# Kernel optimization log

Measured on AMD Instinct MI355X. Metric: run time of the kernel, lower is better.

Reference implementation:

```python
import jax, jax.numpy as jnp
import numpy as np

LOG_SCALE_INIT = float(np.log(10.0))


def lorentz_linear(x, W, b, log_scale):
    # nonlin (gelu) -> linear -> Lorentz time/space renormalization
    y = jax.nn.gelu(x) @ W.T + b
    time = jax.nn.sigmoid(y[..., :1]) * jnp.exp(log_scale) + 1.1
    nar = y[..., 1:]
    denom = jnp.clip(jnp.sum(nar * nar, axis=-1, keepdims=True), 1e-8, None)
    scale = (time * time - 1.0) / denom
    return jnp.concatenate([time, nar * jnp.sqrt(scale)], axis=-1)


def ffn_lorentz(x, W1, b1, s1, W2, b2, s2):
    return lorentz_linear(lorentz_linear(x, W1, b1, s1), W2, b2, s2) + x


def knn_indices(x, k):
    # x: (B,N,C). KNN on detached features (as in ViG dense_knn_matrix).
    xs = jax.lax.stop_gradient(x)
    sq = jnp.sum(xs * xs, axis=-1)  # (B,N)
    d = sq[:, :, None] + sq[:, None, :] - 2.0 * jnp.einsum('bnc,bmc->bnm', xs, xs)
    _, idx = jax.lax.top_k(-d, k)  # (B,N,k) nearest (includes self)
    return idx


def graph_conv(x, Wg, bg, sg, k):
    # Max-relative graph conv with Lorentz linear. x: (B,N,C)
    idx = knn_indices(x, k)
    xj = jax.vmap(lambda xb, ib: xb[ib])(x, idx)  # (B,N,k,C) gather
    msg = jnp.max(xj - x[:, :, None, :], axis=2)  # (B,N,C)
    h = jnp.concatenate([x, msg], axis=-1)        # (B,N,2C)
    return lorentz_linear(h, Wg, bg, sg)


def setup_inputs() -> dict:
    key = jax.random.key(0)
    ks = jax.random.split(key, 8)
    B, C, H, W = 8, 192, 56, 56
    x = jax.random.normal(ks[0], (B, C, H, W), dtype=jnp.float32)
    def lin(k_, fin, fout):
        return jax.random.normal(k_, (fout, fin), dtype=jnp.float32) * 0.02
    p = {
        'x': x,
        'W1': lin(ks[1], C, C), 'b1': jnp.zeros((C,), jnp.float32), 's1': jnp.float32(LOG_SCALE_INIT),
        'W2': lin(ks[2], C, C), 'b2': jnp.zeros((C,), jnp.float32), 's2': jnp.float32(LOG_SCALE_INIT),
        'Wg': lin(ks[3], 2 * C, C), 'bg': jnp.zeros((C,), jnp.float32), 'sg': jnp.float32(LOG_SCALE_INIT),
        'W3': lin(ks[4], C, C), 'b3': jnp.zeros((C,), jnp.float32), 's3': jnp.float32(LOG_SCALE_INIT),
        'W4': lin(ks[5], C, C), 'b4': jnp.zeros((C,), jnp.float32), 's4': jnp.float32(LOG_SCALE_INIT),
        'k': 9,
    }
    return p


def reference(x, W1, b1, s1, W2, b2, s2, Wg, bg, sg, W3, b3, s3, W4, b4, s4, k):
    B, C, H, W = x.shape
    xn = x.reshape(B, C, H * W).transpose(0, 2, 1)  # (B,N,C) == rearrange b c (h w) 1 -> b (h w) c
    shortcut = xn
    xn = ffn_lorentz(xn, W1, b1, s1, W2, b2, s2)
    xn = graph_conv(xn, Wg, bg, sg, k)
    xn = ffn_lorentz(xn, W3, b3, s3, W4, b4, s4)
    xn = xn + shortcut  # drop_path = 0 -> identity
    return xn.transpose(0, 2, 1).reshape(B, C, H, W)
```

## Files before the change

### kernel.cpp

```cpp
#include <hip/hip_runtime.h>
#include <math.h>

#define NB   8
#define NC   192
#define NPIX 3136
#define NPAD 3200
#define GRID_LL (NB*98)
#define NIT  25
#define NSP  8
#define GRID_KNN (NB*NIT*NSP)
#define GRID_MSG (NB*196)
#define FINF 3.4e38f

typedef _Float16 f16x8 __attribute__((ext_vector_type(8)));
typedef float   f32x16 __attribute__((ext_vector_type(16)));

__device__ __forceinline__ float gelu_f(float x){
    float u = 0.7978845608028654f * (x + 0.044715f * x * x * x);
    return 0.5f * x * (1.0f + tanhf(u));
}

__device__ __forceinline__ unsigned pack_hi(float a, float b){
    union { _Float16 f; unsigned short u; } ha, hb;
    ha.f = (_Float16)a; hb.f = (_Float16)b;
    return (unsigned)ha.u | ((unsigned)hb.u << 16);
}

#define LESS9(da,ia,db,ib) ((da) < (db) || ((da) == (db) && (ia) < (ib)))
#define CSW9(a,ia,b,ib) { bool sw_ = LESS9(b,ib,a,ia); float tf_=(a); int ti_=(ia); \
    (a) = sw_? (b) : (a); (ia) = sw_? (ib) : (ia); (b) = sw_? tf_ : (b); (ib) = sw_? ti_ : (ib); }

struct Top9 {
    float d0,d1,d2,d3,d4,d5,d6,d7,d8;
    int   j0,j1,j2,j3,j4,j5,j6,j7,j8;
    __device__ __forceinline__ void init(){
        d0=d1=d2=d3=d4=d5=d6=d7=d8=FINF;
        j0=j1=j2=j3=j4=j5=j6=j7=j8=0x7FFFFFFF;
    }
    __device__ __forceinline__ void insert(float nd, int ni){
        if (!LESS9(nd, ni, d8, j8)) return;
        d8 = nd; j8 = ni;
        CSW9(d7,j7,d8,j8); CSW9(d6,j6,d7,j7); CSW9(d5,j5,d6,j6); CSW9(d4,j4,d5,j5);
        CSW9(d3,j3,d4,j4); CSW9(d2,j2,d3,j3); CSW9(d1,j1,d2,j2); CSW9(d0,j0,d1,j1);
    }
};

__device__ __forceinline__ unsigned f2mono(float e){
    unsigned u = __float_as_uint(e);
    return u ^ ((unsigned)((int)u >> 31) | 0x80000000u);
}
__device__ __forceinline__ float unmono(unsigned m){
    return __uint_as_float(m ^ ((unsigned)(((int)~m) >> 31) | 0x80000000u));
}

#define CSK(a,b) { unsigned h_ = (a) > (b) ? (a) : (b); unsigned l_ = (a) > (b) ? (b) : (a); (a) = h_; (b) = l_; }
#define INSKEY(x_) if ((x_) > t_k11){ t_k11 = (x_); \
    CSK(t_k10,t_k11) CSK(t_k9,t_k10) CSK(t_k8,t_k9) CSK(t_k7,t_k8) \
    CSK(t_k6,t_k7) CSK(t_k5,t_k6) CSK(t_k4,t_k5) CSK(t_k3,t_k4) \
    CSK(t_k2,t_k3) CSK(t_k1,t_k2) CSK(t_k0,t_k1) }

#define KQ(A,Q) { \
    unsigned q0_ = (f2mono(A[4*(Q)+0]) & 0xFFFFF000u) | (unsigned)(jinvb_ - 8*(Q)    ); \
    unsigned q1_ = (f2mono(A[4*(Q)+1]) & 0xFFFFF000u) | (unsigned)(jinvb_ - 8*(Q) - 1); \
    unsigned q2_ = (f2mono(A[4*(Q)+2]) & 0xFFFFF000u) | (unsigned)(jinvb_ - 8*(Q) - 2); \
    unsigned q3_ = (f2mono(A[4*(Q)+3]) & 0xFFFFF000u) | (unsigned)(jinvb_ - 8*(Q) - 3); \
    unsigned qa_ = q0_ > q1_ ? q0_ : q1_; \
    unsigned qb_ = q2_ > q3_ ? q2_ : q3_; \
    unsigned qm_ = qa_ > qb_ ? qa_ : qb_; \
    if (qm_ > t_k11){ INSKEY(q0_) INSKEY(q1_) INSKEY(q2_) INSKEY(q3_) } }

#define AMAX16(A) fmaxf(fmaxf(fmaxf(fmaxf(A[0],A[1]),fmaxf(A[2],A[3])),fmaxf(fmaxf(A[4],A[5]),fmaxf(A[6],A[7]))), \
                        fmaxf(fmaxf(fmaxf(A[8],A[9]),fmaxf(A[10],A[11])),fmaxf(fmaxf(A[12],A[13]),fmaxf(A[14],A[15]))))

#define INSACCK(A,JS) { float am_ = AMAX16(A); \
    if (am_ >= thrf){ int jinvb_ = 4095 - (jg + (JS)*32 + 4*h); \
        KQ(A,0) KQ(A,1) KQ(A,2) KQ(A,3) } }

#define MF(ACC,AO,BO) ACC = __builtin_amdgcn_mfma_f32_32x32x16_f16(AO,BO,ACC,0,0,0);
#define ZERO16 {0,0,0,0,0,0,0,0,0,0,0,0,0,0,0,0}

__global__ __launch_bounds__(256) void wt_kernel(
    const float* __restrict__ W1, const float* __restrict__ W2,
    const float* __restrict__ Wg, const float* __restrict__ W3,
    const float* __restrict__ W4,
    float* __restrict__ W1T, float* __restrict__ W2T, float* __restrict__ WgT,
    float* __restrict__ W3T, float* __restrict__ W4T)
{
    __shared__ float tile[32*33];
    int t = blockIdx.x;
    const float* src; float* dst; int Kin;
    if (t < 36)      { src = W1; dst = W1T; Kin = 192; }
    else if (t < 72) { src = W2; dst = W2T; Kin = 192; t -= 36; }
    else if (t < 144){ src = Wg; dst = WgT; Kin = 384; t -= 72; }
    else if (t < 180){ src = W3; dst = W3T; Kin = 192; t -= 144; }
    else             { src = W4; dst = W4T; Kin = 192; t -= 180; }
    int ntc = Kin >> 5;
    int tr = t / ntc, tc = t - tr*ntc;
    int tid = threadIdx.x;
    {
        int i = tid >> 3, j4 = (tid & 7)*4;
        float4 v = *(const float4*)&src[(size_t)(tr*32 + i)*Kin + tc*32 + j4];
        tile[i*33 + j4+0] = v.x; tile[i*33 + j4+1] = v.y;
        tile[i*33 + j4+2] = v.z; tile[i*33 + j4+3] = v.w;
    }
    __syncthreads();
    {
        int j = tid >> 3, i4 = (tid & 7)*4;
        float4 o = make_float4(tile[(i4+0)*33 + j], tile[(i4+1)*33 + j],
                               tile[(i4+2)*33 + j], tile[(i4+3)*33 + j]);
        *(float4*)&dst[(size_t)(tc*32 + j)*192 + tr*32 + i4] = o;
    }
}

__global__ __launch_bounds__(256) void pad_kernel(
    unsigned short* __restrict__ Xh, unsigned short* __restrict__ S2h)
{
    const int b = blockIdx.x;
    const int tid = threadIdx.x;
    uint4 z = make_uint4(0,0,0,0);
    for (int e = tid; e < 1536; e += 256){
        int r = e / 24, c8 = (e % 24) * 8;
        *(uint4*)&Xh[((size_t)b*NPAD + NPIX + r)*192 + c8] = z;
    }
    if (tid < 64){
        union { _Float16 f; unsigned short u; } p;
        p.f = (_Float16)(-30000.0f);
        S2h[(size_t)b*NPAD + NPIX + tid] = p.u;
    }
}

template<int K, bool DUAL, bool AX, bool AR, bool CONVF>
__global__ __launch_bounds__(256, 4) void ll2_kernel(
    const float* __restrict__ A0, const float* __restrict__ A1,
    const float* __restrict__ WT, const float* __restrict__ bias,
    const float* __restrict__ sptr, const float* __restrict__ Xres,
    const float* __restrict__ Rcm,
    float* __restrict__ OutCM, float* __restrict__ Hrm,
    unsigned short* __restrict__ Xh, unsigned short* __restrict__ S2h,
    float* __restrict__ SQf)
{
    __shared__ float lA[32*36];
    __shared__ float lW[32*196];

    const int tid = threadIdx.x;
    const int tx = tid & 15, ty = tid >> 4;
    const int bid = blockIdx.x;
    const int b  = bid / 98;
    const int n0 = (bid % 98) * 32;

    float acc[2][12];
    #pragma unroll
    for (int mi = 0; mi < 2; ++mi)
        #pragma unroll
        for (int j = 0; j < 12; ++j) acc[mi][j] = 0.f;

    for (int kt = 0; kt < K/32; ++kt){
        {
            int kk = tid >> 3;
            int m4 = (tid & 7) * 4;
            int c  = kt*32 + kk;
            const float* pl;
            if (K > 192 && c >= 192) pl = A1 + ((size_t)b*192 + (c - 192))*NPIX;
            else                     pl = A0 + ((size_t)b*192 + c)*NPIX;
            float4 v = *(const float4*)&pl[n0 + m4];
            v.x = gelu_f(v.x); v.y = gelu_f(v.y); v.z = gelu_f(v.z); v.w = gelu_f(v.w);
            *(float4*)&lA[kk*36 + m4] = v;
        }
        #pragma unroll
        for (int r = 0; r < 6; ++r){
            int e  = tid + r*256;
            int kk = e / 48;
            int c4 = (e - kk*48) * 4;
            float4 v = *(const float4*)&WT[(size_t)(kt*32 + kk)*192 + c4];
            *(float4*)&lW[kk*196 + c4] = v;
        }
        __syncthreads();
        #pragma unroll
        for (int kk = 0; kk < 32; ++kk){
            float2 a2 = *(const float2*)&lA[kk*36 + ty*2];
            float4 w0 = *(const float4*)&lW[kk*196 + tx*12];
            float4 w1 = *(const float4*)&lW[kk*196 + tx*12 + 4];
            float4 w2 = *(const float4*)&lW[kk*196 + tx*12 + 8];
            float aw[2]  = {a2.x, a2.y};
            float wv[12] = {w0.x,w0.y,w0.z,w0.w, w1.x,w1.y,w1.z,w1.w, w2.x,w2.y,w2.z,w2.w};
            #pragma unroll
            for (int mi = 0; mi < 2; ++mi)
                #pragma unroll
                for (int j = 0; j < 12; ++j)
                    acc[mi][j] = fmaf(aw[mi], wv[j], acc[mi][j]);
        }
        __syncthreads();
    }

    const int lane = tid & 63;
    float es = expf(sptr[0]);
    float bv[12];
    #pragma unroll
    for (int q = 0; q < 3; ++q){
        float4 t4 = *(const float4*)&bias[tx*12 + q*4];
        bv[q*4+0] = t4.x; bv[q*4+1] = t4.y; bv[q*4+2] = t4.z; bv[q*4+3] = t4.w;
    }
    #pragma unroll
    for (int mi = 0; mi < 2; ++mi){
        float part = 0.f;
        #pragma unroll
        for (int j = 0; j < 12; ++j){
            float y = acc[mi][j] + bv[j];
            acc[mi][j] = y;
            if (!(tx == 0 && j == 0)) part += y * y;
        }
        #pragma unroll
        for (int m = 1; m < 16; m <<= 1) part += __shfl_xor(part, m, 64);
        float y0   = __shfl(acc[mi][0], lane & 48, 64);
        float tval = es / (1.f + expf(-y0)) + 1.1f;
        float denom = fmaxf(part, 1e-8f);
        float sca  = (tval*tval - 1.f) / denom;
        float sqs  = sqrtf(sca);
        #pragma unroll
        for (int j = 0; j < 12; ++j){
            float o = acc[mi][j] * sqs;
            if (tx == 0 && j == 0) o = tval;
            acc[mi][j] = o;
        }
    }
    if (AX){
        #pragma unroll
        for (int j = 0; j < 12; ++j){
            int c = tx*12 + j;
            float2 xv = *(const float2*)&Xres[((size_t)b*192 + c)*NPIX + n0 + ty*2];
            acc[0][j] += xv.x; acc[1][j] += xv.y;
        }
    }
    if (AR){
        #pragma unroll
        for (int j = 0; j < 12; ++j){
            int c = tx*12 + j;
            float2 rv = *(const float2*)&Rcm[((size_t)b*192 + c)*NPIX + n0 + ty*2];
            acc[0][j] += rv.x; acc[1][j] += rv.y;
        }
    }
    #pragma unroll
    for (int j = 0; j < 12; ++j){
        int c = tx*12 + j;
        *(float2*)&OutCM[((size_t)b*192 + c)*NPIX + n0 + ty*2] = make_float2(acc[0][j], acc[1][j]);
    }
    if (DUAL){
        #pragma unroll
        for (int mi = 0; mi < 2; ++mi){
            #pragma unroll
            for (int q = 0; q < 3; ++q){
                float4 o = make_float4(acc[mi][q*4+0], acc[mi][q*4+1], acc[mi][q*4+2], acc[mi][q*4+3]);
                *(float4*)&Hrm[((size_t)b*NPIX + n0 + ty*2 + mi)*192 + tx*12 + q*4] = o;
            }
        }
    }
    if (CONVF){
        #pragma unroll
        for (int mi = 0; mi < 2; ++mi){
            int row = n0 + ty*2 + mi;
            float s = 0.f;
            #pragma unroll
            for (int j = 0; j < 12; ++j) s = fmaf(acc[mi][j], acc[mi][j], s);
            #pragma unroll
            for (int m = 1; m < 16; m <<= 1) s += __shfl_xor(s, m, 64);
            #pragma unroll
            for (int q = 0; q < 3; ++q){
                uint2 hv;
                hv.x = pack_hi(acc[mi][q*4+0], acc[mi][q*4+1]);
                hv.y = pack_hi(acc[mi][q*4+2], acc[mi][q*4+3]);
                *(uint2*)&Xh[((size_t)b*NPAD + row)*192 + tx*12 + q*4] = hv;
            }
            if (tx == 0){
                SQf[(size_t)b*NPIX + row] = s;
                union { _Float16 f; unsigned short u; } hh;
                hh.f = (_Float16)(-0.5f * s);
                S2h[(size_t)b*NPAD + row] = hh.u;
            }
        }
    }
}

__global__ __launch_bounds__(256) __attribute__((amdgpu_waves_per_eu(2))) void knn_kernel(
    const unsigned short* __restrict__ Xh, const unsigned short* __restrict__ S2h,
    unsigned* __restrict__ PK)
{
    __shared__ uint4 lds[1280];

    const int tid  = threadIdx.x;
    const int lane = tid & 63;
    const int w    = tid >> 6;
    const int l31  = lane & 31;
    const int h    = lane >> 5;
    const int bid  = blockIdx.x;
    const int b    = bid & 7;
    const int t2   = bid >> 3;
    const int itile = t2 >> 3;
    const int sp    = t2 & 7;
    const int i0    = itile * 128;
    const int g0 = (sp*25)/NSP, g1 = ((sp+1)*25)/NSP;
    const size_t rowb = (size_t)b * NPAD;

    unsigned t_k0=0,t_k1=0,t_k2=0,t_k3=0,t_k4=0,t_k5=0,
             t_k6=0,t_k7=0,t_k8=0,t_k9=0,t_k10=0,t_k11=0;
    float thrf = -FINF;

    for (int g = g0; g < g1; ++g){
        const int jg = g*128;
        f32x16 acc0 = ZERO16, acc1 = ZERO16, acc2 = ZERO16, acc3 = ZERO16;

        for (int kc = 0; kc < 6; ++kc){
            __syncthreads();
            #pragma unroll
            for (int rr = 0; rr < 4; ++rr){
                int u   = tid + rr*256;
                int arr = u >> 9;
                int rs  = (u >> 2) & 127;
                int seg = u & 3;
                int row = (arr == 0) ? (jg + rs) : (i0 + rs);
                uint4 v = *(const uint4*)&Xh[(rowb + row)*192 + kc*32 + seg*8];
                lds[arr*640 + rs*5 + seg] = v;
            }
            __syncthreads();
            #pragma unroll
            for (int ks = 0; ks < 2; ++ks){
                int kq  = ks*2 + h;
                int rb  = l31*5 + kq;
                f16x8 bh = __builtin_bit_cast(f16x8, lds[640 + w*160 + rb]);
                f16x8 a0h = __builtin_bit_cast(f16x8, lds[  0 + rb]);
                f16x8 a1h = __builtin_bit_cast(f16x8, lds[160 + rb]);
                f16x8 a2h = __builtin_bit_cast(f16x8, lds[320 + rb]);
                f16x8 a3h = __builtin_bit_cast(f16x8, lds[480 + rb]);
                MF(acc0, a0h, bh)
                MF(acc1, a1h, bh)
                MF(acc2, a2h, bh)
                MF(acc3, a3h, bh)
            }
        }

        {
            unsigned m  = (h == 0) ? 0xFFFFFFFFu : 0u;
            unsigned om = 0x3C00u & m;
            f16x8 one = __builtin_bit_cast(f16x8, make_uint4(om, 0, 0, 0));
            unsigned s0 = (unsigned)S2h[rowb + jg +  0 + l31];
            unsigned s1 = (unsigned)S2h[rowb + jg + 32 + l31];
            unsigned s2 = (unsigned)S2h[rowb + jg + 64 + l31];
            unsigned s3 = (unsigned)S2h[rowb + jg + 96 + l31];
            f16x8 a;
            a = __builtin_bit_cast(f16x8, make_uint4(s0 & m, 0,0,0)); MF(acc0, a, one)
            a = __builtin_bit_cast(f16x8, make_uint4(s1 & m, 0,0,0)); MF(acc1, a, one)
            a = __builtin_bit_cast(f16x8, make_uint4(s2 & m, 0,0,0)); MF(acc2, a, one)
            a = __builtin_bit_cast(f16x8, make_uint4(s3 & m, 0,0,0)); MF(acc3, a, one)
        }

        INSACCK(acc0, 0)
        INSACCK(acc1, 1)
        INSACCK(acc2, 2)
        INSACCK(acc3, 3)
        thrf = (t_k11 != 0u) ? unmono(t_k11 & 0xFFFFF000u) : -FINF;
    }

    #define MRGK(Kk) { unsigned ok_ = __shfl((int)(Kk), lane ^ 32, 64); \
                      if (lane < 32) { INSKEY((unsigned)ok_) } }
    MRGK(t_k0) MRGK(t_k1) MRGK(t_k2) MRGK(t_k3) MRGK(t_k4) MRGK(t_k5)
    MRGK(t_k6) MRGK(t_k7) MRGK(t_k8) MRGK(t_k9) MRGK(t_k10) MRGK(t_k11)

    if (lane < 32){
        size_t po = ((size_t)(t2*8 + b)*128 + (size_t)w*32 + l31)*12;
        PK[po+ 0] = t_k0;  PK[po+ 1] = t_k1;  PK[po+ 2] = t_k2;  PK[po+ 3] = t_k3;
        PK[po+ 4] = t_k4;  PK[po+ 5] = t_k5;  PK[po+ 6] = t_k6;  PK[po+ 7] = t_k7;
        PK[po+ 8] = t_k8;  PK[po+ 9] = t_k9;  PK[po+10] = t_k10; PK[po+11] = t_k11;
    }
}

__global__ __launch_bounds__(256) void merge_msg_kernel(
    const float* __restrict__ H, const float* __restrict__ SQf,
    const unsigned* __restrict__ PK, float* __restrict__ Msg)
{
    __shared__ float liX[16*196];
    __shared__ unsigned kv[1600];
    __shared__ float cd[256];
    __shared__ int   cidx[256];
    __shared__ int   fidx[144];

    const int tid = threadIdx.x;
    const int bid = blockIdx.x;
    const int b  = bid / 196;
    const int i0 = (bid % 196) * 16;
    const int base = b * NPIX;

    #pragma unroll
    for (int k = 0; k < 3; ++k){
        int f = tid + k*256;
        int r = f / 48, c4 = f % 48;
        *(float4*)&liX[r*196 + c4*4] = *(const float4*)&H[(size_t)(base + i0 + r)*192 + c4*4];
    }
    if (tid < 128){
        int r = tid >> 3, sp = tid & 7;
        int i = i0 + r;
        size_t po = ((size_t)(((i>>7)*NSP + sp)*8 + b)*128 + (i & 127))*12;
        #pragma unroll
        for (int q = 0; q < 3; ++q)
            *(uint4*)&kv[r*100 + sp*12 + q*4] = *(const uint4*)&PK[po + q*4];
    }
    __syncthreads();

    if (tid < 16){
        int r = tid;
        int h0=0,h1=0,h2=0,h3=0,h4=0,h5=0,h6=0,h7=0;
        #pragma unroll
        for (int p = 0; p < 16; ++p){
            unsigned bk = 0; int bs = 0;
#define HEADC(SP,HV) { \
            unsigned k_ = (HV < 12) ? kv[r*100 + SP*12 + HV] : 0u; \
            bool bt_ = k_ > bk; \
            bk = bt_? k_ : bk; bs = bt_? SP : bs; }
            HEADC(0,h0) HEADC(1,h1) HEADC(2,h2) HEADC(3,h3)
            HEADC(4,h4) HEADC(5,h5) HEADC(6,h6) HEADC(7,h7)
#undef HEADC
            cidx[r*16 + p] = 4095 - (int)(bk & 0xFFFu);
            h0 += (bs==0); h1 += (bs==1); h2 += (bs==2); h3 += (bs==3);
            h4 += (bs==4); h5 += (bs==5); h6 += (bs==6); h7 += (bs==7);
        }
    }
    __syncthreads();

    {
        int r = tid >> 4, p = tid & 15;
        int j = cidx[r*16 + p];
        const float* hj = &H[(size_t)(base + j)*192];
        float dot = 0.f;
        #pragma unroll
        for (int q = 0; q < 48; ++q){
            float4 xv = *(const float4*)&liX[r*196 + q*4];
            float4 yv = *(const float4*)&hj[q*4];
            dot = fmaf(xv.x,yv.x, fmaf(xv.y,yv.y, fmaf(xv.z,yv.z, fmaf(xv.w,yv.w, dot))));
        }
        cd[r*16 + p] = SQf[base + j] - 2.f*dot;
    }
    __syncthreads();

    if (tid < 16){
        int r = tid;
        Top9 m; m.init();
        #pragma unroll
        for (int c = 0; c < 16; ++c) m.insert(cd[r*16 + c], cidx[r*16 + c]);
        fidx[r*9+0]=m.j0; fidx[r*9+1]=m.j1; fidx[r*9+2]=m.j2; fidx[r*9+3]=m.j3;
        fidx[r*9+4]=m.j4; fidx[r*9+5]=m.j5; fidx[r*9+6]=m.j6; fidx[r*9+7]=m.j7;
        fidx[r*9+8]=m.j8;
    }
    __syncthreads();

    int rr = tid & 15, part = tid >> 4;
    int ii = i0 + rr;
    int nbr[9];
    #pragma unroll
    for (int e = 0; e < 9; ++e) nbr[e] = fidx[rr*9 + e];
    #pragma unroll
    for (int q = 0; q < 3; ++q){
        float4 mv = make_float4(-FINF, -FINF, -FINF, -FINF);
        #pragma unroll
        for (int e = 0; e < 9; ++e){
            float4 v = *(const float4*)&H[(size_t)(base + nbr[e])*192 + part*12 + q*4];
            mv.x = fmaxf(mv.x, v.x); mv.y = fmaxf(mv.y, v.y);
            mv.z = fmaxf(mv.z, v.z); mv.w = fmaxf(mv.w, v.w);
        }
        float4 xi = *(const float4*)&liX[rr*196 + part*12 + q*4];
        float m0 = mv.x - xi.x, m1 = mv.y - xi.y, m2 = mv.z - xi.z, m3 = mv.w - xi.w;
        int c = part*12 + q*4;
        Msg[((size_t)b*192 + c+0)*NPIX + ii] = m0;
        Msg[((size_t)b*192 + c+1)*NPIX + ii] = m1;
        Msg[((size_t)b*192 + c+2)*NPIX + ii] = m2;
        Msg[((size_t)b*192 + c+3)*NPIX + ii] = m3;
    }
}

extern "C" void kernel_launch(void* const* d_in, const int* in_sizes, int n_in,
                              void* d_out, int out_size, void* d_ws, size_t ws_size,
                              hipStream_t stream)
{
    const float* x  = (const float*)d_in[0];
    const float* W1 = (const float*)d_in[1];
    const float* b1 = (const float*)d_in[2];
    const float* s1 = (const float*)d_in[3];
    const float* W2 = (const float*)d_in[4];
    const float* b2 = (const float*)d_in[5];
    const float* s2 = (const float*)d_in[6];
    const float* Wg = (const float*)d_in[7];
    const float* bg = (const float*)d_in[8];
    const float* sg = (const float*)d_in[9];
    const float* W3 = (const float*)d_in[10];
    const float* b3 = (const float*)d_in[11];
    const float* s3 = (const float*)d_in[12];
    const float* W4 = (const float*)d_in[13];
    const float* b4 = (const float*)d_in[14];
    const float* s4 = (const float*)d_in[15];

    const size_t PL = (size_t)25088*192;
    float* Hrm  = (float*)d_ws;
    float* X1cm = Hrm  + PL;
    float* T1cm = X1cm + PL;
    float* X2cm = T1cm + PL;
    float* MXr  = X2cm + PL;
    unsigned short* Xh = (unsigned short*)MXr;
    float* Msg = MXr;
    unsigned short* S2h = (unsigned short*)(MXr + PL);
    float* SQf = (float*)(S2h + (size_t)NB*NPAD);
    float* W1T = SQf + (size_t)NB*NPIX;
    float* W2T = W1T + 36864;
    float* WgT = W2T + 36864;
    float* W3T = WgT + 73728;
    float* W4T = W3T + 36864;
    unsigned* PK = (unsigned*)X2cm;
    float* out = (float*)d_out;

    wt_kernel<<<216, 256, 0, stream>>>(W1, W2, Wg, W3, W4, W1T, W2T, WgT, W3T, W4T);
    pad_kernel<<<NB, 256, 0, stream>>>(Xh, S2h);
    ll2_kernel<192, false, false, false, false><<<GRID_LL, 256, 0, stream>>>(x,    x,    W1T, b1, s1, nullptr, nullptr, T1cm, nullptr, nullptr, nullptr, nullptr);
    ll2_kernel<192, true , true , false, true ><<<GRID_LL, 256, 0, stream>>>(T1cm, T1cm, W2T, b2, s2, x,       nullptr, X1cm, Hrm, Xh, S2h, SQf);
    knn_kernel<<<GRID_KNN, 256, 0, stream>>>(Xh, S2h, PK);
    merge_msg_kernel<<<GRID_MSG, 256, 0, stream>>>(Hrm, SQf, PK, Msg);
    ll2_kernel<384, false, false, false, false><<<GRID_LL, 256, 0, stream>>>(X1cm, Msg,  WgT, bg, sg, nullptr, nullptr, X2cm, nullptr, nullptr, nullptr, nullptr);
    ll2_kernel<192, false, false, false, false><<<GRID_LL, 256, 0, stream>>>(X2cm, X2cm, W3T, b3, s3, nullptr, nullptr, T1cm, nullptr, nullptr, nullptr, nullptr);
    ll2_kernel<192, false, true , true , false><<<GRID_LL, 256, 0, stream>>>(T1cm, T1cm, W4T, b4, s4, x,       X2cm,    out,  nullptr, nullptr, nullptr, nullptr);
}
```

Measured before the change: 501.3 us.

## Move post-KNN Lorentz linears to split-fp16 MFMA kernels with row-major activations

Adds an MFMA-based Lorentz linear kernel that uses hi/lo fp16 splitting (three MFMAs per step) to keep near-fp32 accuracy, and uses it for the graph-conv, W3 and W4 layers in place of the scalar fp32 ll2 kernel. Intermediate activations move to row-major layout, and the message kernel now writes row-major float4 instead of strided channel-major scalars. The W3 output is stored pre-gelu'd and split into fp16 hi/lo so the next layer can load it directly. This trades extra MFMA work and a weight-split pre-pass for removing the slow FMA GEMMs, and accepts some precision risk from the fp16 split.

```diff
diff --git a/kernel.cpp b/kernel.cpp
--- a/kernel.cpp
+++ b/kernel.cpp
@@ -5,7 +5,8 @@
 #define NC   192
 #define NPIX 3136
 #define NPAD 3200
-#define GRID_LL (NB*98)
+#define NMT  98
+#define GRID_LL (NB*NMT)
 #define NIT  25
 #define NSP  8
 #define GRID_KNN (NB*NIT*NSP)
@@ -19,11 +20,11 @@
     float u = 0.7978845608028654f * (x + 0.044715f * x * x * x);
     return 0.5f * x * (1.0f + tanhf(u));
 }
-
+__device__ __forceinline__ unsigned short h2u(_Float16 v){
+    union { _Float16 f; unsigned short u; } c; c.f = v; return c.u;
+}
 __device__ __forceinline__ unsigned pack_hi(float a, float b){
-    union { _Float16 f; unsigned short u; } ha, hb;
-    ha.f = (_Float16)a; hb.f = (_Float16)b;
-    return (unsigned)ha.u | ((unsigned)hb.u << 16);
+    return (unsigned)h2u((_Float16)a) | ((unsigned)h2u((_Float16)b) << 16);
 }
 
 #define LESS9(da,ia,db,ib) ((da) < (db) || ((da) == (db) && (ia) < (ib)))
@@ -81,25 +82,17 @@
 
 __global__ __launch_bounds__(256) void wt_kernel(
     const float* __restrict__ W1, const float* __restrict__ W2,
-    const float* __restrict__ Wg, const float* __restrict__ W3,
-    const float* __restrict__ W4,
-    float* __restrict__ W1T, float* __restrict__ W2T, float* __restrict__ WgT,
-    float* __restrict__ W3T, float* __restrict__ W4T)
+    float* __restrict__ W1T, float* __restrict__ W2T)
 {
     __shared__ float tile[32*33];
     int t = blockIdx.x;
-    const float* src; float* dst; int Kin;
-    if (t < 36)      { src = W1; dst = W1T; Kin = 192; }
-    else if (t < 72) { src = W2; dst = W2T; Kin = 192; t -= 36; }
-    else if (t < 144){ src = Wg; dst = WgT; Kin = 384; t -= 72; }
-    else if (t < 180){ src = W3; dst = W3T; Kin = 192; t -= 144; }
-    else             { src = W4; dst = W4T; Kin = 192; t -= 180; }
-    int ntc = Kin >> 5;
-    int tr = t / ntc, tc = t - tr*ntc;
+    const float* src; float* dst;
+    if (t < 36){ src = W1; dst = W1T; } else { src = W2; dst = W2T; t -= 36; }
+    int tr = t / 6, tc = t - tr*6;
     int tid = threadIdx.x;
     {
         int i = tid >> 3, j4 = (tid & 7)*4;
-        float4 v = *(const float4*)&src[(size_t)(tr*32 + i)*Kin + tc*32 + j4];
+        float4 v = *(const float4*)&src[(size_t)(tr*32 + i)*192 + tc*32 + j4];
         tile[i*33 + j4+0] = v.x; tile[i*33 + j4+1] = v.y;
         tile[i*33 + j4+2] = v.z; tile[i*33 + j4+3] = v.w;
     }
@@ -112,6 +105,23 @@
     }
 }
 
+__global__ __launch_bounds__(256) void wt16_kernel(
+    const float* __restrict__ Wg, const float* __restrict__ W3,
+    const float* __restrict__ W4,
+    unsigned short* __restrict__ Wh, unsigned short* __restrict__ Wl)
+{
+    int i = blockIdx.x*256 + threadIdx.x;
+    if (i >= 147456) return;
+    const float* src; int off;
+    if (i < 73728)       { src = Wg; off = i; }
+    else if (i < 110592) { src = W3; off = i - 73728; }
+    else                 { src = W4; off = i - 110592; }
+    float w = src[off];
+    _Float16 hi = (_Float16)w;
+    Wh[i] = h2u(hi);
+    Wl[i] = h2u((_Float16)(w - (float)hi));
+}
+
 __global__ __launch_bounds__(256) void pad_kernel(
     unsigned short* __restrict__ Xh, unsigned short* __restrict__ S2h)
 {
@@ -129,12 +139,11 @@
     }
 }
 
-template<int K, bool DUAL, bool AX, bool AR, bool CONVF>
+template<int K, bool WCM, bool DUAL, bool AX, bool CONVF>
 __global__ __launch_bounds__(256, 4) void ll2_kernel(
     const float* __restrict__ A0, const float* __restrict__ A1,
     const float* __restrict__ WT, const float* __restrict__ bias,
     const float* __restrict__ sptr, const float* __restrict__ Xres,
-    const float* __restrict__ Rcm,
     float* __restrict__ OutCM, float* __restrict__ Hrm,
     unsigned short* __restrict__ Xh, unsigned short* __restrict__ S2h,
     float* __restrict__ SQf)
@@ -145,8 +154,8 @@
     const int tid = threadIdx.x;
     const int tx = tid & 15, ty = tid >> 4;
     const int bid = blockIdx.x;
-    const int b  = bid / 98;
-    const int n0 = (bid % 98) * 32;
+    const int b  = bid / NMT;
+    const int n0 = (bid % NMT) * 32;
 
     float acc[2][12];
     #pragma unroll
@@ -231,18 +240,12 @@
             acc[0][j] += xv.x; acc[1][j] += xv.y;
         }
     }
-    if (AR){
+    if (WCM){
         #pragma unroll
         for (int j = 0; j < 12; ++j){
             int c = tx*12 + j;
-            float2 rv = *(const float2*)&Rcm[((size_t)b*192 + c)*NPIX + n0 + ty*2];
-            acc[0][j] += rv.x; acc[1][j] += rv.y;
-        }
-    }
-    #pragma unroll
-    for (int j = 0; j < 12; ++j){
-        int c = tx*12 + j;
-        *(float2*)&OutCM[((size_t)b*192 + c)*NPIX + n0 + ty*2] = make_float2(acc[0][j], acc[1][j]);
+            *(float2*)&OutCM[((size_t)b*192 + c)*NPIX + n0 + ty*2] = make_float2(acc[0][j], acc[1][j]);
+        }
     }
     if (DUAL){
         #pragma unroll
@@ -272,10 +275,146 @@
             }
             if (tx == 0){
                 SQf[(size_t)b*NPIX + row] = s;
-                union { _Float16 f; unsigned short u; } hh;
-                hh.f = (_Float16)(-0.5f * s);
-                S2h[(size_t)b*NPAD + row] = hh.u;
+                S2h[(size_t)b*NPAD + row] = h2u((_Float16)(-0.5f * s));
             }
+        }
+    }
+}
+
+template<int K, int AMODE, bool ESPL, bool EF32, bool AXCM, bool ARRM, bool OUTCM>
+__global__ __launch_bounds__(192) void mll_kernel(
+    const unsigned short* __restrict__ Ash, const unsigned short* __restrict__ Asl,
+    const float* __restrict__ Af0, const float* __restrict__ Af1,
+    const unsigned short* __restrict__ Wh, const unsigned short* __restrict__ Wl,
+    const float* __restrict__ bias, const float* __restrict__ sptr,
+    const float* __restrict__ Xcm, const float* __restrict__ Rrm,
+    float* __restrict__ OutF,
+    unsigned short* __restrict__ Oh, unsigned short* __restrict__ Ol)
+{
+    __shared__ float psum[3][32], y0v[32];
+    const int tid = threadIdx.x;
+    const int w = tid >> 6, lane = tid & 63, l31 = lane & 31, h = lane >> 5;
+    const int bid = blockIdx.x;
+    const int b = bid / NMT, mt = bid % NMT;
+    const int row0 = mt*32;
+    const int nb = w*64;
+    const size_t arow = (size_t)b*NPIX + row0 + l31;
+    const int c0 = nb + l31, c1 = nb + 32 + l31;
+
+    f32x16 acc0 = ZERO16, acc1 = ZERO16;
+
+    #pragma unroll
+    for (int ks = 0; ks < K/16; ++ks){
+        const int kb = ks*16 + h*8;
+        f16x8 ah, al;
+        if (AMODE == 0){
+            ah = __builtin_bit_cast(f16x8, *(const uint4*)&Ash[arow*192 + kb]);
+            al = __builtin_bit_cast(f16x8, *(const uint4*)&Asl[arow*192 + kb]);
+        } else {
+            const float* src;
+            if (AMODE == 2) src = (ks < 12) ? (Af0 + arow*192 + kb) : (Af1 + arow*192 + (kb - 192));
+            else            src = Af0 + arow*192 + kb;
+            float4 f0 = *(const float4*)src;
+            float4 f1 = *(const float4*)(src + 4);
+            float g[8] = {f0.x,f0.y,f0.z,f0.w,f1.x,f1.y,f1.z,f1.w};
+            #pragma unroll
+            for (int e = 0; e < 8; ++e){
+                float gg = gelu_f(g[e]);
+                _Float16 hi = (_Float16)gg;
+                ah[e] = hi;
+                al[e] = (_Float16)(gg - (float)hi);
+            }
+        }
+        f16x8 wh0 = __builtin_bit_cast(f16x8, *(const uint4*)&Wh[(size_t)c0*K + kb]);
+        f16x8 wl0 = __builtin_bit_cast(f16x8, *(const uint4*)&Wl[(size_t)c0*K + kb]);
+        f16x8 wh1 = __builtin_bit_cast(f16x8, *(const uint4*)&Wh[(size_t)c1*K + kb]);
+        f16x8 wl1 = __builtin_bit_cast(f16x8, *(const uint4*)&Wl[(size_t)c1*K + kb]);
+        MF(acc0, ah, wh0) MF(acc0, al, wh0) MF(acc0, ah, wl0)
+        MF(acc1, ah, wh1) MF(acc1, al, wh1) MF(acc1, ah, wl1)
+    }
+
+    const float es = expf(sptr[0]);
+    const float bv0 = bias[c0], bv1 = bias[c1];
+    float o0[16], o1[16], p[16];
+    #pragma unroll
+    for (int r = 0; r < 16; ++r){
+        o0[r] = acc0[r] + bv0;
+        o1[r] = acc1[r] + bv1;
+        p[r] = o0[r]*o0[r] + o1[r]*o1[r];
+    }
+    #pragma unroll
+    for (int m = 1; m < 32; m <<= 1){
+        #pragma unroll
+        for (int r = 0; r < 16; ++r) p[r] += __shfl_xor(p[r], m, 64);
+    }
+    if (l31 == 0){
+        #pragma unroll
+        for (int r = 0; r < 16; ++r){
+            int row = (r&3) + 8*(r>>2) + 4*h;
+            float v = p[r];
+            if (w == 0){ v -= o0[r]*o0[r]; y0v[row] = o0[r]; }
+            psum[w][row] = v;
+        }
+    }
+    __syncthreads();
+    #pragma unroll
+    for (int r = 0; r < 16; ++r){
+        int row = (r&3) + 8*(r>>2) + 4*h;
+        float S = psum[0][row] + psum[1][row] + psum[2][row];
+        float y0 = y0v[row];
+        float tval = es / (1.f + expf(-y0)) + 1.1f;
+        float denom = fmaxf(S, 1e-8f);
+        float sqs = sqrtf((tval*tval - 1.f)/denom);
+        o0[r] *= sqs; o1[r] *= sqs;
+        if (w == 0 && l31 == 0) o0[r] = tval;
+    }
+    if (AXCM){
+        #pragma unroll
+        for (int p4 = 0; p4 < 4; ++p4){
+            float4 xv0 = *(const float4*)&Xcm[((size_t)b*192 + c0)*NPIX + row0 + 8*p4 + 4*h];
+            float4 xv1 = *(const float4*)&Xcm[((size_t)b*192 + c1)*NPIX + row0 + 8*p4 + 4*h];
+            o0[4*p4+0] += xv0.x; o0[4*p4+1] += xv0.y; o0[4*p4+2] += xv0.z; o0[4*p4+3] += xv0.w;
+            o1[4*p4+0] += xv1.x; o1[4*p4+1] += xv1.y; o1[4*p4+2] += xv1.z; o1[4*p4+3] += xv1.w;
+        }
+    }
+    if (ARRM){
+        #pragma unroll
+        for (int r = 0; r < 16; ++r){
+            int row = (r&3) + 8*(r>>2) + 4*h;
+            o0[r] += Rrm[((size_t)b*NPIX + row0 + row)*192 + c0];
+            o1[r] += Rrm[((size_t)b*NPIX + row0 + row)*192 + c1];
+        }
+    }
+    if (OUTCM){
+        #pragma unroll
+        for (int p4 = 0; p4 < 4; ++p4){
+            *(float4*)&OutF[((size_t)b*192 + c0)*NPIX + row0 + 8*p4 + 4*h] =
+                make_float4(o0[4*p4+0], o0[4*p4+1], o0[4*p4+2], o0[4*p4+3]);
+            *(float4*)&OutF[((size_t)b*192 + c1)*NPIX + row0 + 8*p4 + 4*h] =
+                make_float4(o1[4*p4+0], o1[4*p4+1], o1[4*p4+2], o1[4*p4+3]);
+        }
+    }
+    if (EF32){
+        #pragma unroll
+        for (int r = 0; r < 16; ++r){
+            int row = (r&3) + 8*(r>>2) + 4*h;
+            OutF[((size_t)b*NPIX + row0 + row)*192 + c0] = o0[r];
+            OutF[((size_t)b*NPIX + row0 + row)*192 + c1] = o1[r];
+        }
+    }
+    if (ESPL){
+        #pragma unroll
+        for (int r = 0; r < 16; ++r){
+            int row = (r&3) + 8*(r>>2) + 4*h;
+            size_t o = ((size_t)b*NPIX + row0 + row)*192;
+            float g0 = gelu_f(o0[r]);
+            _Float16 h0 = (_Float16)g0;
+            Oh[o + c0] = h2u(h0);
+            Ol[o + c0] = h2u((_Float16)(g0 - (float)h0));
+            float g1 = gelu_f(o1[r]);
+            _Float16 h1 = (_Float16)g1;
+            Oh[o + c1] = h2u(h1);
+            Ol[o + c1] = h2u((_Float16)(g1 - (float)h1));
         }
     }
 }
@@ -450,7 +589,7 @@
     }
     __syncthreads();
 
-    int rr = tid & 15, part = tid >> 4;
+    int rr = tid >> 4, part = tid & 15;
     int ii = i0 + rr;
     int nbr[9];
     #pragma unroll
@@ -465,12 +604,8 @@
             mv.z = fmaxf(mv.z, v.z); mv.w = fmaxf(mv.w, v.w);
         }
         float4 xi = *(const float4*)&liX[rr*196 + part*12 + q*4];
-        float m0 = mv.x - xi.x, m1 = mv.y - xi.y, m2 = mv.z - xi.z, m3 = mv.w - xi.w;
-        int c = part*12 + q*4;
-        Msg[((size_t)b*192 + c+0)*NPIX + ii] = m0;
-        Msg[((size_t)b*192 + c+1)*NPIX + ii] = m1;
-        Msg[((size_t)b*192 + c+2)*NPIX + ii] = m2;
-        Msg[((size_t)b*192 + c+3)*NPIX + ii] = m3;
+        *(float4*)&Msg[(size_t)(base + ii)*192 + part*12 + q*4] =
+            make_float4(mv.x - xi.x, mv.y - xi.y, mv.z - xi.z, mv.w - xi.w);
     }
 }
 
@@ -494,32 +629,44 @@
     const float* W4 = (const float*)d_in[13];
     const float* b4 = (const float*)d_in[14];
     const float* s4 = (const float*)d_in[15];
-
-    const size_t PL = (size_t)25088*192;
-    float* Hrm  = (float*)d_ws;
-    float* X1cm = Hrm  + PL;
-    float* T1cm = X1cm + PL;
-    float* X2cm = T1cm + PL;
-    float* MXr  = X2cm + PL;
-    unsigned short* Xh = (unsigned short*)MXr;
-    float* Msg = MXr;
-    unsigned short* S2h = (unsigned short*)(MXr + PL);
+    float* ws = (float*)d_ws;
+    float* out = (float*)d_out;
+
+    const size_t NE = (size_t)NB*NPIX*192;
+    float* T1cm = ws;
+    float* Msg  = ws;
+    float* Hrm = ws + NE;
+    unsigned short* GT3h = (unsigned short*)Hrm;
+    unsigned short* GT3l = GT3h + NE;
+    float* X2f = ws + 2*NE;
+    unsigned short* Xh  = (unsigned short*)(ws + 3*NE);
+    unsigned short* S2h = Xh + (size_t)NB*NPAD*192;
     float* SQf = (float*)(S2h + (size_t)NB*NPAD);
-    float* W1T = SQf + (size_t)NB*NPIX;
+    unsigned* PK = (unsigned*)(SQf + (size_t)NB*NPIX);
+    float* W1T = (float*)(PK + (size_t)GRID_KNN*128*12);
     float* W2T = W1T + 36864;
-    float* WgT = W2T + 36864;
-    float* W3T = WgT + 73728;
-    float* W4T = W3T + 36864;
-    unsigned* PK = (unsigned*)X2cm;
-    float* out = (float*)d_out;
-
-    wt_kernel<<<216, 256, 0, stream>>>(W1, W2, Wg, W3, W4, W1T, W2T, WgT, W3T, W4T);
+    unsigned short* Wh16 = (unsigned short*)(W2T + 36864);
+    unsigned short* Wl16 = Wh16 + 147456;
+    const unsigned short* Wgh = Wh16,          *Wgl = Wl16;
+    const unsigned short* W3h = Wh16 + 73728,  *W3l = Wl16 + 73728;
+    const unsigned short* W4h = Wh16 + 110592, *W4l = Wl16 + 110592;
+
+    wt_kernel<<<72, 256, 0, stream>>>(W1, W2, W1T, W2T);
+    wt16_kernel<<<576, 256, 0, stream>>>(Wg, W3, W4, Wh16, Wl16);
     pad_kernel<<<NB, 256, 0, stream>>>(Xh, S2h);
-    ll2_kernel<192, false, false, false, false><<<GRID_LL, 256, 0, stream>>>(x,    x,    W1T, b1, s1, nullptr, nullptr, T1cm, nullptr, nullptr, nullptr, nullptr);
-    ll2_kernel<192, true , true , false, true ><<<GRID_LL, 256, 0, stream>>>(T1cm, T1cm, W2T, b2, s2, x,       nullptr, X1cm, Hrm, Xh, S2h, SQf);
+    ll2_kernel<192, true , false, false, false><<<GRID_LL, 256, 0, stream>>>(
+        x, x, W1T, b1, s1, nullptr, T1cm, nullptr, nullptr, nullptr, nullptr);
+    ll2_kernel<192, false, true , true , true ><<<GRID_LL, 256, 0, stream>>>(
+        T1cm, T1cm, W2T, b2, s2, x, nullptr, Hrm, Xh, S2h, SQf);
     knn_kernel<<<GRID_KNN, 256, 0, stream>>>(Xh, S2h, PK);
     merge_msg_kernel<<<GRID_MSG, 256, 0, stream>>>(Hrm, SQf, PK, Msg);
-    ll2_kernel<384, false, false, false, false><<<GRID_LL, 256, 0, stream>>>(X1cm, Msg,  WgT, bg, sg, nullptr, nullptr, X2cm, nullptr, nullptr, nullptr, nullptr);
-    ll2_kernel<192, false, false, false, false><<<GRID_LL, 256, 0, stream>>>(X2cm, X2cm, W3T, b3, s3, nullptr, nullptr, T1cm, nullptr, nullptr, nullptr, nullptr);
-    ll2_kernel<192, false, true , true , false><<<GRID_LL, 256, 0, stream>>>(T1cm, T1cm, W4T, b4, s4, x,       X2cm,    out,  nullptr, nullptr, nullptr, nullptr);
-}
+    mll_kernel<384,2,false,true ,false,false,false><<<GRID_LL, 192, 0, stream>>>(
+        nullptr, nullptr, Hrm, Msg, Wgh, Wgl, bg, sg, nullptr, nullptr,
+        X2f, nullptr, nullptr);
+    mll_kernel<192,1,true ,false,false,false,false><<<GRID_LL, 192, 0, stream>>>(
+        nullptr, nullptr, X2f, nullptr, W3h, W3l, b3, s3, nullptr, nullptr,
+        nullptr, GT3h, GT3l);
+    mll_kernel<192,0,false,false,true ,true ,true ><<<GRID_LL, 192, 0, stream>>>(
+        GT3h, GT3l, nullptr, nullptr, W4h, W4l, b4, s4, x, X2f,
+        out, nullptr, nullptr);
+}
```

Result: faster. 447.6 us (-10.7%).
